# Kernel tuning notes

Hardware: AMD Instinct MI355X
Metric: run time of the kernel (lower is better)

The kernel has to match this reference:

```python
import jax, jax.numpy as jnp
import numpy as np

WS = 8         # window size (square)
SHIFT = 4      # shift size
NUM_HEADS = 8

def _layernorm(x, g, b, eps=1e-5):
    m = x.mean(-1, keepdims=True)
    v = ((x - m) ** 2).mean(-1, keepdims=True)
    return (x - m) / jnp.sqrt(v + eps) * g + b

def _rel_index():
    # relative_position_index for num_frames_q = num_frames_kv = 1 (d-term is 0)
    ch = np.arange(WS)
    coords = np.stack(np.meshgrid(ch, ch, indexing='ij'))      # (2, WS, WS)
    flat = coords.reshape(2, -1)                                 # (2, N)
    rel = flat[:, :, None] - flat[:, None, :]                    # (2, N, N)
    idx = (rel[0] + WS - 1) * (2 * WS - 1) + (rel[1] + WS - 1)   # (N, N)
    return jnp.asarray(idx, dtype=jnp.int32)

def setup_inputs() -> dict:
    key = jax.random.key(0)
    ks = jax.random.split(key, 16)
    B, D, H, W, C = 2, 2, 256, 256, 256
    hid = 4 * C
    nW = (H // WS) * (W // WS)
    N = WS * WS
    f = jax.random.normal
    return {
        'x': f(ks[0], (B, D, H, W, C), jnp.float32),
        'mask_matrix': f(ks[1], (nW, N, N), jnp.float32),
        'g1': jnp.ones((C,), jnp.float32),
        'b1': jnp.zeros((C,), jnp.float32),
        'qw': f(ks[2], (C, C), jnp.float32) * 0.02,
        'qb': jnp.zeros((C,), jnp.float32),
        'kvw': f(ks[3], (2 * C, C), jnp.float32) * 0.02,
        'kvb': jnp.zeros((2 * C,), jnp.float32),
        'pw': f(ks[4], (C, C), jnp.float32) * 0.02,
        'pb': jnp.zeros((C,), jnp.float32),
        'bias_table': f(ks[5], ((2 * WS - 1) ** 2, NUM_HEADS), jnp.float32) * 0.02,
        'g2': jnp.ones((C,), jnp.float32),
        'b2': jnp.zeros((C,), jnp.float32),
        'w1': f(ks[6], (hid, C), jnp.float32) * 0.02,
        'bi1': jnp.zeros((hid,), jnp.float32),
        'w2': f(ks[7], (C, hid), jnp.float32) * 0.02,
        'bi2': jnp.zeros((C,), jnp.float32),
    }

def reference(x, mask_matrix, g1, b1, qw, qb, kvw, kvb, pw, pb, bias_table, g2, b2, w1, bi1, w2, bi2):
    B, D, H, W, C = x.shape
    h = NUM_HEADS
    d = C // h
    N = WS * WS
    nH, nWc = H // WS, W // WS
    nwin = nH * nWc

    shortcut = x[:, 0]                       # (B, H, W, C)  (frame 0)
    xn = _layernorm(x, g1, b1)
    xs = jnp.roll(xn, (-SHIFT, -SHIFT), axis=(2, 3))   # cyclic shift

    # window partition: (B, D, H, W, C) -> (B*nwin, D, N, C)
    win = xs.reshape(B, D, nH, WS, nWc, WS, C)
    win = win.transpose(0, 2, 4, 1, 3, 5, 6).reshape(B * nwin, D, N, C)
    q_in = win[:, 0]                          # (B_, N, C) query = frame 0
    kv_in = win[:, 1]                         # (B_, N, C) kv    = frame 1

    q = (q_in @ qw.T + qb).reshape(-1, N, h, d).transpose(0, 2, 1, 3) * (d ** -0.5)
    kv = (kv_in @ kvw.T + kvb).reshape(-1, N, 2, h, d).transpose(2, 0, 3, 1, 4)
    k, v = kv[0], kv[1]                       # (B_, h, N, d)

    attn = jnp.einsum('bhnd,bhmd->bhnm', q, k)            # (B_, h, N, N)
    bias = bias_table[_rel_index()]                        # (N, N, h)
    attn = attn + bias.transpose(2, 0, 1)[None]
    attn = attn.reshape(B, nwin, h, N, N) + mask_matrix[None, :, None]
    attn = jax.nn.softmax(attn.reshape(-1, h, N, N), axis=-1)

    out = jnp.einsum('bhnm,bhmd->bhnd', attn, v)          # (B_, h, N, d)
    out = out.transpose(0, 2, 1, 3).reshape(-1, N, C)
    out = out @ pw.T + pb + q_in                           # residual inside attn

    # window reverse: (B*nwin, N, C) -> (B, H, W, C)
    out = out.reshape(B, nH, nWc, WS, WS, C).transpose(0, 1, 3, 2, 4, 5).reshape(B, H, W, C)
    out = jnp.roll(out, (SHIFT, SHIFT), axis=(1, 2))

    x1 = shortcut + out
    y = _layernorm(x1, g2, b2)
    y = jax.nn.gelu(y @ w1.T + bi1, approximate=False) @ w2.T + bi2
    return x1 + y
```

## Files before the change

### kernel.cpp

```cpp
#include <hip/hip_runtime.h>
#include <hip/hip_bf16.h>
#include <math.h>

#define SHIFT_ 4

typedef __attribute__((ext_vector_type(8))) short bh8;
typedef __attribute__((ext_vector_type(4))) short sh4;
typedef __attribute__((ext_vector_type(4))) float f4;
typedef __attribute__((ext_vector_type(8))) __bf16 bf8t;

static __device__ __forceinline__ f4 mfma16(bh8 a, bh8 b, f4 c){
  return __builtin_amdgcn_mfma_f32_16x16x32_bf16(
    __builtin_bit_cast(bf8t, a), __builtin_bit_cast(bf8t, b), c, 0, 0, 0);
}
static __device__ __forceinline__ unsigned short f2b(float f){
  unsigned u = __builtin_bit_cast(unsigned, f);
  u += 0x7fffu + ((u >> 16) & 1u);
  return (unsigned short)(u >> 16);
}
static __device__ __forceinline__ float b2f(unsigned short h){
  return __builtin_bit_cast(float, ((unsigned)h) << 16);
}
static __device__ __forceinline__ unsigned cvt_pk_bf16(float lo, float hi){
  unsigned r;
  asm("v_cvt_pk_bf16_f32 %0, %1, %2" : "=v"(r) : "v"(lo), "v"(hi));
  return r;
}
static __device__ __forceinline__ float gelu_f(float hv){
  float u = hv * (1.5957691216f + 0.0713548162f * hv * hv);
  return hv * __builtin_amdgcn_rcpf(1.f + __expf(-u));
}
static __device__ __forceinline__ void glds16(const unsigned short* g, unsigned short* l){
  __builtin_amdgcn_global_load_lds(
    (const __attribute__((address_space(1))) unsigned int*)g,
    (__attribute__((address_space(3))) unsigned int*)l, 16, 0, 0);
}

__global__ __launch_bounds__(256) void prep_w(
    const float* __restrict__ qw, const float* __restrict__ kvw,
    const float* __restrict__ pw, const float* __restrict__ w1,
    const float* __restrict__ w2, unsigned short* __restrict__ wb){
  int i = blockIdx.x * 256 + threadIdx.x;
  float v;
  if      (i < 65536)  v = qw[i] * 0.17677669529663687f;
  else if (i < 196608) v = kvw[i - 65536];
  else if (i < 262144) v = pw[i - 196608];
  else if (i < 524288) v = w1[i - 262144];
  else                 v = w2[i - 524288];
  wb[i] = f2b(v);
}

__global__ __launch_bounds__(256) void ln1_win(
    const float* __restrict__ x, const float* __restrict__ g1,
    const float* __restrict__ b1,
    unsigned short* __restrict__ q_in, unsigned short* __restrict__ kv_in){
  int rid  = blockIdx.x * 4 + (threadIdx.x >> 6);
  int lane = threadIdx.x & 63;
  int d    = rid >> 17;
  int rem  = rid & 131071;
  int w = rem >> 6, n = rem & 63;
  int b = w >> 10, hb = (w >> 5) & 31, wbk = w & 31;
  int sh = (hb * 8 + (n >> 3) + SHIFT_) & 255;
  int sw = (wbk * 8 + (n & 7) + SHIFT_) & 255;
  const float* src = x + ((((size_t)(b * 2 + d)) * 256 + sh) * 256 + sw) * 256;
  float4 v = *(const float4*)(src + lane * 4);
  float s  = v.x + v.y + v.z + v.w;
  float ss = v.x * v.x + v.y * v.y + v.z * v.z + v.w * v.w;
  #pragma unroll
  for (int off = 1; off < 64; off <<= 1){ s += __shfl_xor(s, off); ss += __shfl_xor(ss, off); }
  float m    = s * (1.f / 256.f);
  float rstd = rsqrtf(ss * (1.f / 256.f) - m * m + 1e-5f);
  int c = lane * 4;
  float4 g  = *(const float4*)(g1 + c);
  float4 bb = *(const float4*)(b1 + c);
  sh4 o;
  o.x = (short)f2b((v.x - m) * rstd * g.x + bb.x);
  o.y = (short)f2b((v.y - m) * rstd * g.y + bb.y);
  o.z = (short)f2b((v.z - m) * rstd * g.z + bb.z);
  o.w = (short)f2b((v.w - m) * rstd * g.w + bb.w);
  unsigned short* dst = (d == 0 ? q_in : kv_in) + (size_t)rem * 256 + c;
  *(sh4*)dst = o;
}

__global__ __launch_bounds__(512, 4) void qkv_gemm(
    const unsigned short* __restrict__ q_in, const unsigned short* __restrict__ kv_in,
    const unsigned short* __restrict__ wpack,
    const float* __restrict__ qbias, const float* __restrict__ kvbias,
    unsigned short* __restrict__ qo, unsigned short* __restrict__ ko,
    unsigned short* __restrict__ vo){
  __shared__ unsigned short sA[128][64];
  __shared__ unsigned short sB[256][64];
  int m0 = blockIdx.x * 128;
  int tid = threadIdx.x, lane = tid & 63, wid = tid >> 6;
  int wm = wid >> 2, wn = wid & 3;
  int llo = lane & 15, lhi = lane >> 4;
  int lr = lane >> 3, lc = (lane & 7) * 8;
  const f4 FZ = {0.f, 0.f, 0.f, 0.f};
  for (int nt = 0; nt < 3; nt++){
    const unsigned short* A  = (nt == 0) ? q_in : kv_in;
    const unsigned short* Wt = wpack + nt * 65536;
    const float* bias = (nt == 0) ? qbias : kvbias + (nt - 1) * 256;
    unsigned short* outb = (nt == 0) ? qo : (nt == 1 ? ko : vo);
    float bscale = (nt == 0) ? 0.17677669529663687f : 1.f;
    f4 acc[4][4];
    for (int i = 0; i < 4; i++) for (int j = 0; j < 4; j++) acc[i][j] = FZ;
    for (int t = 0; t < 4; t++){
      int k0 = t * 64;
      #pragma unroll
      for (int c = 0; c < 2; c++){
        int rr = wid * 16 + c * 8;
        glds16(A + (size_t)(m0 + rr + lr) * 256 + k0 + lc, &sA[rr][0]);
      }
      #pragma unroll
      for (int c = 0; c < 4; c++){
        int rb = wid * 32 + c * 8;
        glds16(Wt + (size_t)(rb + lr) * 256 + k0 + lc, &sB[rb][0]);
      }
      __syncthreads();
      #pragma unroll
      for (int ks = 0; ks < 2; ks++){
        bh8 a[4], b[4];
        #pragma unroll
        for (int mi = 0; mi < 4; mi++) a[mi] = *(const bh8*)&sA[wm * 64 + mi * 16 + llo][ks * 32 + lhi * 8];
        #pragma unroll
        for (int nj = 0; nj < 4; nj++) b[nj] = *(const bh8*)&sB[wn * 64 + nj * 16 + llo][ks * 32 + lhi * 8];
        #pragma unroll
        for (int mi = 0; mi < 4; mi++)
          #pragma unroll
          for (int nj = 0; nj < 4; nj++)
            acc[mi][nj] = mfma16(b[nj], a[mi], acc[mi][nj]);
      }
      __syncthreads();
    }
    #pragma unroll
    for (int nj = 0; nj < 4; nj++){
      int cb = wn * 64 + nj * 16 + lhi * 4;
      float4 bv = *(const float4*)(bias + cb);
      #pragma unroll
      for (int mi = 0; mi < 4; mi++){
        int row = m0 + wm * 64 + mi * 16 + llo;
        float f0 = acc[mi][nj][0] + bv.x * bscale;
        float f1 = acc[mi][nj][1] + bv.y * bscale;
        float f2 = acc[mi][nj][2] + bv.z * bscale;
        float f3 = acc[mi][nj][3] + bv.w * bscale;
        uint2 p;
        p.x = cvt_pk_bf16(f0, f1);
        p.y = cvt_pk_bf16(f2, f3);
        *(uint2*)(outb + (size_t)row * 256 + cb) = p;
      }
    }
  }
}

__global__ __launch_bounds__(256, 2) void attn_k(
    const unsigned short* __restrict__ q, const unsigned short* __restrict__ k,
    const unsigned short* __restrict__ v, const float* __restrict__ mask,
    const float* __restrict__ bias_table, unsigned short* __restrict__ aout){
  __shared__ unsigned short sMask[64][72];
  __shared__ unsigned short sVT[128][72];
  __shared__ unsigned short sP[4][64][72];
  __shared__ float sBias[4][225];
  int bid = blockIdx.x;
  int w = bid >> 1, hg = bid & 1;
  int tid = threadIdx.x, lane = tid & 63, wid = tid >> 6;
  int hd = hg * 4 + wid;
  int llo = lane & 15, lhi = lane >> 4;
  const unsigned short* qp = q + (size_t)w * 64 * 256 + hd * 32;
  const unsigned short* kp = k + (size_t)w * 64 * 256 + hd * 32;
  bh8 af[4], bf[4];
  #pragma unroll
  for (int mi = 0; mi < 4; mi++) af[mi] = *(const bh8*)(qp + (size_t)(mi * 16 + llo) * 256 + lhi * 8);
  #pragma unroll
  for (int nj = 0; nj < 4; nj++) bf[nj] = *(const bh8*)(kp + (size_t)(nj * 16 + llo) * 256 + lhi * 8);
  const float* mrow = mask + (size_t)(w & 1023) * 4096;
  #pragma unroll
  for (int i = 0; i < 2; i++){
    int base = (tid + i * 256) * 8;
    float4 u0 = *(const float4*)(mrow + base);
    float4 u1 = *(const float4*)(mrow + base + 4);
    int rr = base >> 6, cc = base & 63;
    uint4 p;
    p.x = cvt_pk_bf16(u0.x, u0.y); p.y = cvt_pk_bf16(u0.z, u0.w);
    p.z = cvt_pk_bf16(u1.x, u1.y); p.w = cvt_pk_bf16(u1.z, u1.w);
    *(uint4*)&sMask[rr][cc] = p;
  }
  {
    const unsigned short* vp = v + (size_t)w * 64 * 256 + hg * 128;
    #pragma unroll
    for (int it = 0; it < 4; it++){
      int idx = tid + it * 256;
      int n = idx >> 4, dc = (idx & 15) * 8;
      bh8 vv = *(const bh8*)(vp + (size_t)n * 256 + dc);
      #pragma unroll
      for (int j = 0; j < 8; j++) sVT[dc + j][n] = (unsigned short)vv[j];
    }
  }
  for (int i = lane; i < 225; i += 64) sBias[wid][i] = bias_table[i * 8 + hd];
  const f4 FZ = {0.f, 0.f, 0.f, 0.f};
  f4 acc[4][4];
  #pragma unroll
  for (int mi = 0; mi < 4; mi++)
    #pragma unroll
    for (int nj = 0; nj < 4; nj++)
      acc[mi][nj] = mfma16(af[mi], bf[nj], FZ);
  __syncthreads();
  #pragma unroll
  for (int mi = 0; mi < 4; mi++){
    #pragma unroll
    for (int r = 0; r < 4; r++){
      int rr = mi * 16 + lhi * 4 + r;
      int yi = rr >> 3, xi = rr & 7;
      float sv[4]; float mx = -1e30f;
      #pragma unroll
      for (int nj = 0; nj < 4; nj++){
        int cc = nj * 16 + llo;
        int idx = (yi - (cc >> 3) + 7) * 15 + (xi - (cc & 7) + 7);
        sv[nj] = acc[mi][nj][r] + sBias[wid][idx] + b2f(sMask[rr][cc]);
        mx = fmaxf(mx, sv[nj]);
      }
      #pragma unroll
      for (int off = 1; off < 16; off <<= 1) mx = fmaxf(mx, __shfl_xor(mx, off));
      float sum = 0.f;
      #pragma unroll
      for (int nj = 0; nj < 4; nj++){ sv[nj] = __expf(sv[nj] - mx); sum += sv[nj]; }
      #pragma unroll
      for (int off = 1; off < 16; off <<= 1) sum += __shfl_xor(sum, off);
      float inv = __builtin_amdgcn_rcpf(sum);
      #pragma unroll
      for (int nj = 0; nj < 4; nj++) sP[wid][rr][nj * 16 + llo] = f2b(sv[nj] * inv);
    }
  }
  f4 o[4][2];
  for (int mi = 0; mi < 4; mi++) for (int dj = 0; dj < 2; dj++) o[mi][dj] = FZ;
  #pragma unroll
  for (int ks = 0; ks < 2; ks++){
    bh8 pa[4], vb[2];
    #pragma unroll
    for (int mi = 0; mi < 4; mi++) pa[mi] = *(const bh8*)&sP[wid][mi * 16 + llo][ks * 32 + lhi * 8];
    #pragma unroll
    for (int dj = 0; dj < 2; dj++) vb[dj] = *(const bh8*)&sVT[wid * 32 + dj * 16 + llo][ks * 32 + lhi * 8];
    #pragma unroll
    for (int mi = 0; mi < 4; mi++)
      #pragma unroll
      for (int dj = 0; dj < 2; dj++)
        o[mi][dj] = mfma16(pa[mi], vb[dj], o[mi][dj]);
  }
  #pragma unroll
  for (int mi = 0; mi < 4; mi++)
    for (int dj = 0; dj < 2; dj++)
      for (int r = 0; r < 4; r++){
        int rr = mi * 16 + lhi * 4 + r, dd = dj * 16 + llo;
        aout[((size_t)w * 64 + rr) * 256 + hd * 32 + dd] = f2b(o[mi][dj][r]);
      }
}

__global__ __launch_bounds__(512, 4) void pgemm_ln(
    const unsigned short* __restrict__ A, const unsigned short* __restrict__ Wt,
    const float* __restrict__ bias,
    float* __restrict__ outf, const unsigned short* __restrict__ qin,
    const float* __restrict__ xsrc,
    const float* __restrict__ g2, const float* __restrict__ b2,
    unsigned short* __restrict__ xn){
  __shared__ unsigned short sA[128][64];
  __shared__ unsigned short sB[256][64];
  __shared__ float sSum[128][4];
  __shared__ float sSq[128][4];
  __shared__ float sMV[128][2];
  int m0 = blockIdx.x * 128;
  int tid = threadIdx.x, lane = tid & 63, wid = tid >> 6;
  int wm = wid >> 2, wn = wid & 3;
  int llo = lane & 15, lhi = lane >> 4;
  int lr = lane >> 3, lc = (lane & 7) * 8;
  const f4 FZ = {0.f, 0.f, 0.f, 0.f};
  f4 acc[4][4];
  for (int i = 0; i < 4; i++) for (int j = 0; j < 4; j++) acc[i][j] = FZ;
  for (int t = 0; t < 4; t++){
    int k0 = t * 64;
    #pragma unroll
    for (int c = 0; c < 2; c++){
      int rr = wid * 16 + c * 8;
      glds16(A + (size_t)(m0 + rr + lr) * 256 + k0 + lc, &sA[rr][0]);
    }
    #pragma unroll
    for (int c = 0; c < 4; c++){
      int rb = wid * 32 + c * 8;
      glds16(Wt + (size_t)(rb + lr) * 256 + k0 + lc, &sB[rb][0]);
    }
    __syncthreads();
    #pragma unroll
    for (int ks = 0; ks < 2; ks++){
      bh8 a[4], b[4];
      #pragma unroll
      for (int mi = 0; mi < 4; mi++) a[mi] = *(const bh8*)&sA[wm * 64 + mi * 16 + llo][ks * 32 + lhi * 8];
      #pragma unroll
      for (int nj = 0; nj < 4; nj++) b[nj] = *(const bh8*)&sB[wn * 64 + nj * 16 + llo][ks * 32 + lhi * 8];
      #pragma unroll
      for (int mi = 0; mi < 4; mi++)
        #pragma unroll
        for (int nj = 0; nj < 4; nj++)
          acc[mi][nj] = mfma16(a[mi], b[nj], acc[mi][nj]);
    }
    __syncthreads();
  }
  #pragma unroll
  for (int mi = 0; mi < 4; mi++){
    #pragma unroll
    for (int r = 0; r < 4; r++){
      int row = m0 + wm * 64 + mi * 16 + lhi * 4 + r;
      int w = row >> 6, n = row & 63;
      int b = w >> 10, hb = (w >> 5) & 31, wbk = w & 31;
      int hh = (hb * 8 + (n >> 3) + SHIFT_) & 255;
      int ww = (wbk * 8 + (n & 7) + SHIFT_) & 255;
      const float* sc = xsrc + (((size_t)(b * 2) * 256 + hh) * 256 + ww) * 256;
      #pragma unroll
      for (int nj = 0; nj < 4; nj++){
        int col = wn * 64 + nj * 16 + llo;
        acc[mi][nj][r] += bias[col] + b2f(qin[(size_t)row * 256 + col]) + sc[col];
      }
    }
  }
  #pragma unroll
  for (int mi = 0; mi < 4; mi++){
    #pragma unroll
    for (int r = 0; r < 4; r++){
      float s = 0.f, sq = 0.f;
      #pragma unroll
      for (int nj = 0; nj < 4; nj++){ float v = acc[mi][nj][r]; s += v; sq += v * v; }
      #pragma unroll
      for (int off = 1; off < 16; off <<= 1){ s += __shfl_xor(s, off); sq += __shfl_xor(sq, off); }
      if (llo == 0){
        int rl = wm * 64 + mi * 16 + lhi * 4 + r;
        sSum[rl][wn] = s; sSq[rl][wn] = sq;
      }
    }
  }
  __syncthreads();
  if (tid < 128){
    float s = sSum[tid][0] + sSum[tid][1] + sSum[tid][2] + sSum[tid][3];
    float q = sSq[tid][0] + sSq[tid][1] + sSq[tid][2] + sSq[tid][3];
    float mean = s * (1.f / 256.f);
    float var  = q * (1.f / 256.f) - mean * mean;
    sMV[tid][0] = mean;
    sMV[tid][1] = rsqrtf(var + 1e-5f);
  }
  __syncthreads();
  float g2v[4], b2v[4];
  #pragma unroll
  for (int nj = 0; nj < 4; nj++){
    int col = wn * 64 + nj * 16 + llo;
    g2v[nj] = g2[col]; b2v[nj] = b2[col];
  }
  #pragma unroll
  for (int mi = 0; mi < 4; mi++){
    #pragma unroll
    for (int r = 0; r < 4; r++){
      int rl = wm * 64 + mi * 16 + lhi * 4 + r;
      int row = m0 + rl;
      float mean = sMV[rl][0], rstd = sMV[rl][1];
      int w = row >> 6, n = row & 63;
      int b = w >> 10, hb = (w >> 5) & 31, wbk = w & 31;
      int hh = (hb * 8 + (n >> 3) + SHIFT_) & 255;
      int ww = (wbk * 8 + (n & 7) + SHIFT_) & 255;
      size_t rbase = (((size_t)b * 256 + hh) * 256 + ww) * 256;
      #pragma unroll
      for (int nj = 0; nj < 4; nj++){
        int col = wn * 64 + nj * 16 + llo;
        float v = acc[mi][nj][r];
        outf[rbase + col] = v;
        xn[rbase + col] = f2b((v - mean) * rstd * g2v[nj] + b2v[nj]);
      }
    }
  }
}

template<int KSTEPS, int EPI, int BIASF>
__global__ __launch_bounds__(256, 3) void mlp_gemm(
    const unsigned short* __restrict__ A, int lda,
    const unsigned short* __restrict__ Bw, int ldb,
    const float* __restrict__ bias,
    unsigned short* __restrict__ outb, int ldo,
    float* __restrict__ outf){
  __shared__ unsigned short sA[128][64];
  __shared__ unsigned short sB[128][64];
  int n0 = blockIdx.x * 128, m0 = blockIdx.y * 128;
  int tid = threadIdx.x, lane = tid & 63, wid = tid >> 6;
  int wm = wid >> 1, wn = wid & 1;
  int llo = lane & 15, lhi = lane >> 4;
  int lr = lane >> 3, lc = (lane & 7) * 8;
  const f4 FZ = {0.f, 0.f, 0.f, 0.f};
  f4 acc[4][4];
  for (int i = 0; i < 4; i++) for (int j = 0; j < 4; j++) acc[i][j] = FZ;

  for (int t = 0; t < KSTEPS; t++){
    int k0 = t * 64;
    #pragma unroll
    for (int c = 0; c < 4; c++){
      int rr = wid * 32 + c * 8 + lr;
      glds16(A  + (size_t)(m0 + rr) * lda + k0 + lc, &sA[wid * 32 + c * 8][0]);
      glds16(Bw + (size_t)(n0 + rr) * ldb + k0 + lc, &sB[wid * 32 + c * 8][0]);
    }
    __syncthreads();
    #pragma unroll
    for (int ks = 0; ks < 2; ks++){
      bh8 a[4], b[4];
      #pragma unroll
      for (int mi = 0; mi < 4; mi++) a[mi] = *(const bh8*)&sA[wm * 64 + mi * 16 + llo][ks * 32 + lhi * 8];
      #pragma unroll
      for (int nj = 0; nj < 4; nj++) b[nj] = *(const bh8*)&sB[wn * 64 + nj * 16 + llo][ks * 32 + lhi * 8];
      #pragma unroll
      for (int mi = 0; mi < 4; mi++)
        #pragma unroll
        for (int nj = 0; nj < 4; nj++){
          if (EPI == 0) acc[mi][nj] = mfma16(b[nj], a[mi], acc[mi][nj]);
          else          acc[mi][nj] = mfma16(a[mi], b[nj], acc[mi][nj]);
        }
    }
    __syncthreads();
  }
  if (EPI == 0){
    #pragma unroll
    for (int nj = 0; nj < 4; nj++){
      int cb = n0 + wn * 64 + nj * 16 + lhi * 4;
      float4 bv = *(const float4*)(bias + cb);
      #pragma unroll
      for (int mi = 0; mi < 4; mi++){
        int row = m0 + wm * 64 + mi * 16 + llo;
        float g0 = gelu_f(acc[mi][nj][0] + bv.x);
        float g1 = gelu_f(acc[mi][nj][1] + bv.y);
        float g2 = gelu_f(acc[mi][nj][2] + bv.z);
        float g3 = gelu_f(acc[mi][nj][3] + bv.w);
        uint2 p;
        p.x = cvt_pk_bf16(g0, g1);
        p.y = cvt_pk_bf16(g2, g3);
        *(uint2*)(outb + (size_t)row * ldo + cb) = p;
      }
    }
  } else {
    #pragma unroll
    for (int mi = 0; mi < 4; mi++)
      #pragma unroll
      for (int nj = 0; nj < 4; nj++){
        int col = n0 + wn * 64 + nj * 16 + llo;
        float bv = BIASF ? bias[col] : 0.f;
        #pragma unroll
        for (int r = 0; r < 4; r++){
          int row = m0 + wm * 64 + mi * 16 + lhi * 4 + r;
          outf[(size_t)row * 256 + col] += acc[mi][nj][r] + bv;
        }
      }
  }
}

extern "C" void kernel_launch(void* const* d_in, const int* in_sizes, int n_in,
                              void* d_out, int out_size, void* d_ws, size_t ws_size,
                              hipStream_t stream){
  const float* x          = (const float*)d_in[0];
  const float* mask       = (const float*)d_in[1];
  const float* g1         = (const float*)d_in[2];
  const float* b1         = (const float*)d_in[3];
  const float* qw         = (const float*)d_in[4];
  const float* qb         = (const float*)d_in[5];
  const float* kvw        = (const float*)d_in[6];
  const float* kvb        = (const float*)d_in[7];
  const float* pw         = (const float*)d_in[8];
  const float* pb         = (const float*)d_in[9];
  const float* bias_table = (const float*)d_in[10];
  const float* g2         = (const float*)d_in[11];
  const float* b2         = (const float*)d_in[12];
  const float* w1         = (const float*)d_in[13];
  const float* bi1        = (const float*)d_in[14];
  const float* w2         = (const float*)d_in[15];
  const float* bi2        = (const float*)d_in[16];
  float* out = (float*)d_out;
  char* ws = (char*)d_ws;
  const long long MB = 1048576LL;
  unsigned short* wb    = (unsigned short*)(ws);
  unsigned short* q_in  = (unsigned short*)(ws + (long long)(1.5 * MB));
  unsigned short* kv_in = (unsigned short*)(ws + (long long)(65.5 * MB));
  unsigned short* qbuf  = (unsigned short*)(ws + (long long)(129.5 * MB));
  unsigned short* kbuf  = (unsigned short*)(ws + (long long)(193.5 * MB));
  unsigned short* vbuf  = (unsigned short*)(ws + (long long)(257.5 * MB));
  unsigned short* aoutb = kv_in;
  unsigned short* xn    = vbuf;
  unsigned short* Hh    = q_in;

  prep_w<<<3072, 256, 0, stream>>>(qw, kvw, pw, w1, w2, wb);
  ln1_win<<<65536, 256, 0, stream>>>(x, g1, b1, q_in, kv_in);
  qkv_gemm<<<1024, 512, 0, stream>>>(q_in, kv_in, wb, qb, kvb, qbuf, kbuf, vbuf);
  attn_k<<<4096, 256, 0, stream>>>(qbuf, kbuf, vbuf, mask, bias_table, aoutb);
  pgemm_ln<<<1024, 512, 0, stream>>>(aoutb, wb + 196608, pb, out, q_in, x,
                                     g2, b2, xn);
  const unsigned short* w1b = wb + 262144;
  const unsigned short* w2b = wb + 524288;
  for (int h = 0; h < 2; h++){
    const long long R = (long long)h * 65536;
    mlp_gemm<4, 0, 0><<<dim3(8, 512), 256, 0, stream>>>(xn + R * 256, 256, w1b, 256,
                                                        bi1, Hh, 1024, nullptr);
    mlp_gemm<16, 1, 1><<<dim3(2, 512), 256, 0, stream>>>(Hh, 1024, w2b, 1024,
                                                         bi2, nullptr, 0, out + R * 256);
  }
}
```

Before: 876.6 us.

## Split LayerNorm2 out of projection GEMM and vectorize epilogue via transposed MFMA

The projection GEMM now swaps the MFMA operands so each lane holds four consecutive columns of one row. This lets the residual/bias epilogue use float4 loads and stores instead of scattered scalar accesses. The fused LayerNorm2 (cross-wave reduction through shared memory, extra barriers) is moved into a separate row-per-wavefront kernel. In exchange, the float x1 result must be re-read from global memory and there is one more kernel launch.

```diff
diff --git a/kernel.cpp b/kernel.cpp
--- a/kernel.cpp
+++ b/kernel.cpp
@@ -254,18 +254,13 @@
       }
 }
 
-__global__ __launch_bounds__(512, 4) void pgemm_ln(
+__global__ __launch_bounds__(512, 4) void pgemm(
     const unsigned short* __restrict__ A, const unsigned short* __restrict__ Wt,
     const float* __restrict__ bias,
     float* __restrict__ outf, const unsigned short* __restrict__ qin,
-    const float* __restrict__ xsrc,
-    const float* __restrict__ g2, const float* __restrict__ b2,
-    unsigned short* __restrict__ xn){
+    const float* __restrict__ xsrc){
   __shared__ unsigned short sA[128][64];
   __shared__ unsigned short sB[256][64];
-  __shared__ float sSum[128][4];
-  __shared__ float sSq[128][4];
-  __shared__ float sMV[128][2];
   int m0 = blockIdx.x * 128;
   int tid = threadIdx.x, lane = tid & 63, wid = tid >> 6;
   int wm = wid >> 2, wn = wid & 3;
@@ -298,79 +293,58 @@
       for (int mi = 0; mi < 4; mi++)
         #pragma unroll
         for (int nj = 0; nj < 4; nj++)
-          acc[mi][nj] = mfma16(a[mi], b[nj], acc[mi][nj]);
+          acc[mi][nj] = mfma16(b[nj], a[mi], acc[mi][nj]);
     }
     __syncthreads();
   }
   #pragma unroll
   for (int mi = 0; mi < 4; mi++){
-    #pragma unroll
-    for (int r = 0; r < 4; r++){
-      int row = m0 + wm * 64 + mi * 16 + lhi * 4 + r;
-      int w = row >> 6, n = row & 63;
-      int b = w >> 10, hb = (w >> 5) & 31, wbk = w & 31;
-      int hh = (hb * 8 + (n >> 3) + SHIFT_) & 255;
-      int ww = (wbk * 8 + (n & 7) + SHIFT_) & 255;
-      const float* sc = xsrc + (((size_t)(b * 2) * 256 + hh) * 256 + ww) * 256;
-      #pragma unroll
-      for (int nj = 0; nj < 4; nj++){
-        int col = wn * 64 + nj * 16 + llo;
-        acc[mi][nj][r] += bias[col] + b2f(qin[(size_t)row * 256 + col]) + sc[col];
-      }
-    }
-  }
-  #pragma unroll
-  for (int mi = 0; mi < 4; mi++){
-    #pragma unroll
-    for (int r = 0; r < 4; r++){
-      float s = 0.f, sq = 0.f;
-      #pragma unroll
-      for (int nj = 0; nj < 4; nj++){ float v = acc[mi][nj][r]; s += v; sq += v * v; }
-      #pragma unroll
-      for (int off = 1; off < 16; off <<= 1){ s += __shfl_xor(s, off); sq += __shfl_xor(sq, off); }
-      if (llo == 0){
-        int rl = wm * 64 + mi * 16 + lhi * 4 + r;
-        sSum[rl][wn] = s; sSq[rl][wn] = sq;
-      }
-    }
-  }
-  __syncthreads();
-  if (tid < 128){
-    float s = sSum[tid][0] + sSum[tid][1] + sSum[tid][2] + sSum[tid][3];
-    float q = sSq[tid][0] + sSq[tid][1] + sSq[tid][2] + sSq[tid][3];
-    float mean = s * (1.f / 256.f);
-    float var  = q * (1.f / 256.f) - mean * mean;
-    sMV[tid][0] = mean;
-    sMV[tid][1] = rsqrtf(var + 1e-5f);
-  }
-  __syncthreads();
-  float g2v[4], b2v[4];
-  #pragma unroll
-  for (int nj = 0; nj < 4; nj++){
-    int col = wn * 64 + nj * 16 + llo;
-    g2v[nj] = g2[col]; b2v[nj] = b2[col];
-  }
-  #pragma unroll
-  for (int mi = 0; mi < 4; mi++){
-    #pragma unroll
-    for (int r = 0; r < 4; r++){
-      int rl = wm * 64 + mi * 16 + lhi * 4 + r;
-      int row = m0 + rl;
-      float mean = sMV[rl][0], rstd = sMV[rl][1];
-      int w = row >> 6, n = row & 63;
-      int b = w >> 10, hb = (w >> 5) & 31, wbk = w & 31;
-      int hh = (hb * 8 + (n >> 3) + SHIFT_) & 255;
-      int ww = (wbk * 8 + (n & 7) + SHIFT_) & 255;
-      size_t rbase = (((size_t)b * 256 + hh) * 256 + ww) * 256;
-      #pragma unroll
-      for (int nj = 0; nj < 4; nj++){
-        int col = wn * 64 + nj * 16 + llo;
-        float v = acc[mi][nj][r];
-        outf[rbase + col] = v;
-        xn[rbase + col] = f2b((v - mean) * rstd * g2v[nj] + b2v[nj]);
-      }
-    }
-  }
+    int row = m0 + wm * 64 + mi * 16 + llo;
+    int w = row >> 6, n = row & 63;
+    int b = w >> 10, hb = (w >> 5) & 31, wbk = w & 31;
+    int hh = (hb * 8 + (n >> 3) + SHIFT_) & 255;
+    int ww = (wbk * 8 + (n & 7) + SHIFT_) & 255;
+    size_t rbase = (((size_t)b * 256 + hh) * 256 + ww) * 256;
+    size_t xbase = (((size_t)(b * 2) * 256 + hh) * 256 + ww) * 256;
+    const unsigned short* qrow = qin + (size_t)row * 256;
+    #pragma unroll
+    for (int nj = 0; nj < 4; nj++){
+      int cb = wn * 64 + nj * 16 + lhi * 4;
+      float4 bv = *(const float4*)(bias + cb);
+      uint2 qv = *(const uint2*)(qrow + cb);
+      float4 xv = *(const float4*)(xsrc + xbase + cb);
+      float4 o;
+      o.x = acc[mi][nj][0] + bv.x + b2f((unsigned short)(qv.x & 0xffff)) + xv.x;
+      o.y = acc[mi][nj][1] + bv.y + b2f((unsigned short)(qv.x >> 16))    + xv.y;
+      o.z = acc[mi][nj][2] + bv.z + b2f((unsigned short)(qv.y & 0xffff)) + xv.z;
+      o.w = acc[mi][nj][3] + bv.w + b2f((unsigned short)(qv.y >> 16))    + xv.w;
+      *(float4*)(outf + rbase + cb) = o;
+    }
+  }
+}
+
+__global__ __launch_bounds__(256) void ln2_k(
+    const float* __restrict__ x1, const float* __restrict__ g2,
+    const float* __restrict__ b2, unsigned short* __restrict__ xn){
+  int rid  = blockIdx.x * 4 + (threadIdx.x >> 6);
+  int lane = threadIdx.x & 63;
+  const float* xr = x1 + (size_t)rid * 256;
+  float4 v = *(const float4*)(xr + lane * 4);
+  float s  = v.x + v.y + v.z + v.w;
+  float ss = v.x * v.x + v.y * v.y + v.z * v.z + v.w * v.w;
+  #pragma unroll
+  for (int off = 1; off < 64; off <<= 1){ s += __shfl_xor(s, off); ss += __shfl_xor(ss, off); }
+  float m    = s * (1.f / 256.f);
+  float rstd = rsqrtf(ss * (1.f / 256.f) - m * m + 1e-5f);
+  int c = lane * 4;
+  float4 g  = *(const float4*)(g2 + c);
+  float4 bb = *(const float4*)(b2 + c);
+  sh4 o;
+  o.x = (short)f2b((v.x - m) * rstd * g.x + bb.x);
+  o.y = (short)f2b((v.y - m) * rstd * g.y + bb.y);
+  o.z = (short)f2b((v.z - m) * rstd * g.z + bb.z);
+  o.w = (short)f2b((v.w - m) * rstd * g.w + bb.w);
+  *(sh4*)(xn + (size_t)rid * 256 + c) = o;
 }
 
 template<int KSTEPS, int EPI, int BIASF>
@@ -488,8 +462,8 @@
   ln1_win<<<65536, 256, 0, stream>>>(x, g1, b1, q_in, kv_in);
   qkv_gemm<<<1024, 512, 0, stream>>>(q_in, kv_in, wb, qb, kvb, qbuf, kbuf, vbuf);
   attn_k<<<4096, 256, 0, stream>>>(qbuf, kbuf, vbuf, mask, bias_table, aoutb);
-  pgemm_ln<<<1024, 512, 0, stream>>>(aoutb, wb + 196608, pb, out, q_in, x,
-                                     g2, b2, xn);
+  pgemm<<<1024, 512, 0, stream>>>(aoutb, wb + 196608, pb, out, q_in, x);
+  ln2_k<<<32768, 256, 0, stream>>>(out, g2, b2, xn);
   const unsigned short* w1b = wb + 262144;
   const unsigned short* w2b = wb + 524288;
   for (int h = 0; h < 2; h++){
```

Result: faster. 776.8 us (-11.4%).
